# Kernel tuning notes

Measured on AMD Instinct MI355X. Metric: run time of the kernel, lower is better.

The kernel has to match this reference:

```python
import jax, jax.numpy as jnp
import numpy as np

B, S, D, H, DFF = 2, 2048, 1024, 16, 4096
DK = D // H
EPS = 1e-6
MASK_FILL = -1.0  # original code uses -1**9 == -1 (precedence bug), NOT -1e9


def layernorm(x, gamma, beta):
    # original: (x - mean) / (std + eps), std unbiased (torch default ddof=1), scalar gamma/beta
    mean = jnp.mean(x, axis=-1, keepdims=True)
    std = jnp.std(x, axis=-1, keepdims=True, ddof=1)
    return gamma * (x - mean) / (std + EPS) + beta


def setup_inputs() -> dict:
    key = jax.random.key(0)
    ks = jax.random.split(key, 12)
    sc = 0.02
    return {
        "x": jax.random.normal(ks[0], (B, S, D), jnp.float32),
        "src_mask": jnp.ones((B, 1, 1, S), jnp.int32),
        "wq": jax.random.normal(ks[1], (D, D), jnp.float32) * sc,
        "bq": jnp.zeros((D,), jnp.float32),
        "wk": jax.random.normal(ks[2], (D, D), jnp.float32) * sc,
        "bk": jnp.zeros((D,), jnp.float32),
        "wv": jax.random.normal(ks[3], (D, D), jnp.float32) * sc,
        "bv": jnp.zeros((D,), jnp.float32),
        "wo": jax.random.normal(ks[4], (D, D), jnp.float32) * sc,
        "bo": jnp.zeros((D,), jnp.float32),
        "w1": jax.random.normal(ks[5], (D, DFF), jnp.float32) * sc,
        "b1": jnp.zeros((DFF,), jnp.float32),
        "w2": jax.random.normal(ks[6], (DFF, D), jnp.float32) * sc,
        "b2": jnp.zeros((D,), jnp.float32),
        "g1": jnp.ones((), jnp.float32),
        "be1": jnp.zeros((), jnp.float32),
        "g2": jnp.ones((), jnp.float32),
        "be2": jnp.zeros((), jnp.float32),
    }


def reference(x, src_mask, wq, bq, wk, bk, wv, bv, wo, bo,
              w1, b1, w2, b2, g1, be1, g2, be2):
    # --- residual 1: pre-LN self-attention ---
    xn = layernorm(x, g1, be1)
    q = (xn @ wq + bq).reshape(B, S, H, DK).transpose(0, 2, 1, 3)  # [B,H,S,DK]
    k = (xn @ wk + bk).reshape(B, S, H, DK).transpose(0, 2, 1, 3)
    v = (xn @ wv + bv).reshape(B, S, H, DK).transpose(0, 2, 1, 3)
    scores = jnp.einsum('bhqd,bhkd->bhqk', q, k) / jnp.sqrt(jnp.float32(DK))
    scores = jnp.where(src_mask == 0, MASK_FILL, scores)
    attn = jax.nn.softmax(scores, axis=-1)
    ctx = jnp.einsum('bhqk,bhkd->bhqd', attn, v)
    ctx = ctx.transpose(0, 2, 1, 3).reshape(B, S, D)
    attn_out = ctx @ wo + bo
    x = x + attn_out  # dropout is identity in eval

    # --- residual 2: pre-LN feed-forward ---
    xn = layernorm(x, g2, be2)
    h = jax.nn.relu(xn @ w1 + b1)
    ff_out = h @ w2 + b2
    return x + ff_out
```

## Files before the change

kernel.cpp:

```cpp
#include <hip/hip_runtime.h>

typedef unsigned short u16;
typedef __bf16 bf16x8 __attribute__((ext_vector_type(8)));
typedef float f32x4 __attribute__((ext_vector_type(4)));
typedef float f32x16 __attribute__((ext_vector_type(16)));

#define AS1U(p) ((__attribute__((address_space(1))) unsigned int*)(p))
#define AS3U(p) ((__attribute__((address_space(3))) unsigned int*)(p))

__device__ __forceinline__ u16 f2bf(float f) {
  union { float f; unsigned int i; } c; c.f = f;
  return (u16)((c.i + 0x7FFFu + ((c.i >> 16) & 1u)) >> 16);
}
__device__ __forceinline__ u16 f2bf_trunc(float f) {
  union { float f; unsigned int i; } c; c.f = f;
  return (u16)(c.i >> 16);
}
__device__ __forceinline__ unsigned cvt_pk_bf16(float lo, float hi) {
  unsigned r;
  asm("v_cvt_pk_bf16_f32 %0, %1, %2" : "=v"(r) : "v"(lo), "v"(hi));
  return r;
}
__device__ __forceinline__ void plswap(unsigned& a, unsigned& b) {
  asm("v_permlane32_swap_b32 %0, %1" : "+v"(a), "+v"(b));
}

template <int OMODE>
__global__ __launch_bounds__(512, 2) void gemm8(
    const u16* __restrict__ A, long lda,
    const u16* __restrict__ B, long ldb,
    void* __restrict__ Cv, long ldc,
    int K, const float* __restrict__ bias,
    const float* __restrict__ res, long ldres, int relu) {
  __shared__ u16 As[2][256 * 64];
  __shared__ u16 Bs[2][256 * 64];
  const int t = threadIdx.x;
  const int w = t >> 6, l = t & 63;
  const int hi = l >> 5, lq = l & 31;
  const int wm = w >> 2, wn = w & 3;
  const long row0 = (long)blockIdx.x * 256;
  const long col0 = (long)blockIdx.y * 256;

  auto stageU = [&](int bb, int unit, int k0) {
    const u16* src = (unit < 2) ? B : A;
    const long ld = (unit < 2) ? ldb : lda;
    const long base0 = (unit < 2) ? col0 : row0;
    u16* dst = (unit < 2) ? &Bs[bb][0] : &As[bb][0];
    const int h = unit & 1;
#pragma unroll
    for (int i = 0; i < 2; i++) {
      int s = t + i * 512;
      int r = h * 128 + (s >> 3), c = s & 7;
      __builtin_amdgcn_global_load_lds(AS1U(src + (base0 + r) * ld + k0 + ((c ^ (r & 7)) * 8)),
                                       AS3U(dst + ((long)(r * 8 + c)) * 8), 16, 0, 0);
    }
  };

  f32x16 acc[4][2] = {};
  const int NT = K >> 6;

  stageU(0, 0, 0); stageU(0, 1, 0); stageU(0, 2, 0); stageU(0, 3, 0);
  if (NT > 1) stageU(1, 0, 64);
  asm volatile("s_waitcnt vmcnt(2)" ::: "memory");
  __builtin_amdgcn_sched_barrier(0);
  __builtin_amdgcn_s_barrier();
  __builtin_amdgcn_sched_barrier(0);

  bf16x8 bfr[2][4];
  for (int tt = 0; tt < NT; tt++) {
    const int cb = tt & 1, nb = cb ^ 1;
    const int kN = (tt + 1) << 6, kN2 = (tt + 2) << 6;
#pragma unroll
    for (int mi = 0; mi < 4; mi++) {
      bf16x8 afr[4];
      {
        const int r = wm * 128 + mi * 32 + lq;
#pragma unroll
        for (int kk = 0; kk < 4; kk++)
          afr[kk] = *(const bf16x8*)&As[cb][(r * 8 + ((kk * 2 + hi) ^ (r & 7))) * 8];
      }
      if (mi == 0) {
#pragma unroll
        for (int nj = 0; nj < 2; nj++) {
          const int r = wn * 64 + nj * 32 + lq;
#pragma unroll
          for (int kk = 0; kk < 4; kk++)
            bfr[nj][kk] = *(const bf16x8*)&Bs[cb][(r * 8 + ((kk * 2 + hi) ^ (r & 7))) * 8];
        }
      }
      if (mi == 0) { if (tt + 1 < NT) stageU(nb, 1, kN); }
      else if (mi == 1) { if (tt + 1 < NT) stageU(nb, 2, kN); }
      else if (mi == 2) { if (tt + 1 < NT) stageU(nb, 3, kN); }
      else {
        if (tt + 2 < NT) stageU(cb, 0, kN2);
        if (tt < NT - 2) asm volatile("s_waitcnt vmcnt(2)" ::: "memory");
        else             asm volatile("s_waitcnt vmcnt(0)" ::: "memory");
      }
      __builtin_amdgcn_sched_barrier(0);
      __builtin_amdgcn_s_barrier();
      __builtin_amdgcn_sched_barrier(0);
      __builtin_amdgcn_s_setprio(1);
#pragma unroll
      for (int kk = 0; kk < 4; kk++)
#pragma unroll
        for (int nj = 0; nj < 2; nj++)
          acc[mi][nj] = __builtin_amdgcn_mfma_f32_32x32x16_bf16(afr[kk], bfr[nj][kk], acc[mi][nj], 0, 0, 0);
      __builtin_amdgcn_s_setprio(0);
      __builtin_amdgcn_sched_barrier(0);
      __builtin_amdgcn_s_barrier();
      __builtin_amdgcn_sched_barrier(0);
    }
  }

#pragma unroll
  for (int nj = 0; nj < 2; nj++) {
    const long gn = col0 + wn * 64 + nj * 32 + lq;
    const float bv = bias ? bias[gn] : 0.0f;
#pragma unroll
    for (int mi = 0; mi < 4; mi++) {
#pragma unroll
      for (int g = 0; g < 16; g++) {
        const long gm = row0 + wm * 128 + mi * 32 + (g & 3) + 8 * (g >> 2) + 4 * hi;
        float v = acc[mi][nj][g] + bv;
        if (relu && v < 0.0f) v = 0.0f;
        if (res) v += res[gm * ldres + gn];
        if (OMODE == 0) ((float*)Cv)[gm * ldc + gn] = v;
        else ((u16*)Cv)[gm * ldc + gn] = f2bf(v);
      }
    }
  }
}

template <int BM, int BN, int BK, int OMODE>
__global__ __launch_bounds__(256) void gemm_bt(
    const u16* __restrict__ A, long lda,
    const u16* __restrict__ B, long ldb,
    void* __restrict__ Cv, long ldc,
    int K, float scale, const float* __restrict__ bias,
    const float* __restrict__ res, long ldres, int relu) {
  constexpr int WN = (BN == 128) ? 64 : 32;
  constexpr int MI = 4, NJ = WN / 16;
  constexpr int KK = BK / 32;
  __shared__ u16 As0[BM * BK], As1[BM * BK];
  __shared__ u16 Bs0[BN * BK], Bs1[BN * BK];
  const int t = threadIdx.x;
  const int w = t >> 6, l = t & 63;
  const int wr = w >> 1, wc = w & 1;
  const int quad = l >> 4, mlo = l & 15;
  const long row0 = (long)blockIdx.x * BM;
  const long col0 = (long)blockIdx.y * BN;

  f32x4 acc[MI][NJ] = {};

  auto stage = [&](u16 (&Ad)[BM * BK], u16 (&Bd)[BN * BK], int k0) {
    if (BK == 32) {
#pragma unroll
      for (int i = 0; i < BM / 64; i++) {
        int s = t + i * 256, r = s >> 2, c = s & 3;
        const u16* g = A + (row0 + r) * lda + k0 + c * 8;
        __builtin_amdgcn_global_load_lds(AS1U(g), AS3U(&Ad[s * 8]), 16, 0, 0);
      }
#pragma unroll
      for (int i = 0; i < BN / 64; i++) {
        int s = t + i * 256, r = s >> 2, c = s & 3;
        const u16* g = B + (col0 + r) * ldb + k0 + c * 8;
        __builtin_amdgcn_global_load_lds(AS1U(g), AS3U(&Bd[s * 8]), 16, 0, 0);
      }
    } else {
#pragma unroll
      for (int i = 0; i < BM / 32; i++) {
        int s = t + i * 256, r = s >> 3, c = s & 7;
        const u16* g = A + (row0 + r) * lda + k0 + (c ^ (r & 7)) * 8;
        __builtin_amdgcn_global_load_lds(AS1U(g), AS3U(&Ad[s * 8]), 16, 0, 0);
      }
#pragma unroll
      for (int i = 0; i < BN / 32; i++) {
        int s = t + i * 256, r = s >> 3, c = s & 7;
        const u16* g = B + (col0 + r) * ldb + k0 + (c ^ (r & 7)) * 8;
        __builtin_amdgcn_global_load_lds(AS1U(g), AS3U(&Bd[s * 8]), 16, 0, 0);
      }
    }
  };
  auto compute = [&](const u16 (&Asr)[BM * BK], const u16 (&Bsr)[BN * BK]) {
#pragma unroll
    for (int kk = 0; kk < KK; kk++) {
      bf16x8 a[MI], b[NJ];
#pragma unroll
      for (int i = 0; i < MI; i++) {
        int r = wr * 64 + i * 16 + mlo;
        a[i] = (BK == 32) ? *(const bf16x8*)&Asr[(r * 4 + quad) * 8]
                          : *(const bf16x8*)&Asr[(r * 8 + ((kk * 4 + quad) ^ (r & 7))) * 8];
      }
#pragma unroll
      for (int j = 0; j < NJ; j++) {
        int r = wc * WN + j * 16 + mlo;
        b[j] = (BK == 32) ? *(const bf16x8*)&Bsr[(r * 4 + quad) * 8]
                          : *(const bf16x8*)&Bsr[(r * 8 + ((kk * 4 + quad) ^ (r & 7))) * 8];
      }
#pragma unroll
      for (int i = 0; i < MI; i++)
#pragma unroll
        for (int j = 0; j < NJ; j++)
          acc[i][j] = __builtin_amdgcn_mfma_f32_16x16x32_bf16(a[i], b[j], acc[i][j], 0, 0, 0);
    }
  };

  stage(As0, Bs0, 0);
  for (int k0 = 0; k0 < K; k0 += 2 * BK) {
    __syncthreads();
    stage(As1, Bs1, k0 + BK);
    compute(As0, Bs0);
    __syncthreads();
    if (k0 + 2 * BK < K) stage(As0, Bs0, k0 + 2 * BK);
    compute(As1, Bs1);
  }

#pragma unroll
  for (int i = 0; i < MI; i++) {
#pragma unroll
    for (int j = 0; j < NJ; j++) {
      const long gn = col0 + wc * WN + j * 16 + mlo;
      const float bv = bias ? bias[gn] : 0.0f;
#pragma unroll
      for (int r = 0; r < 4; r++) {
        const long gm = row0 + wr * 64 + i * 16 + quad * 4 + r;
        float v = acc[i][j][r] * scale + bv;
        if (relu && v < 0.0f) v = 0.0f;
        if (res) v += res[gm * ldres + gn];
        if (OMODE == 0) ((float*)Cv)[gm * ldc + gn] = v;
        else ((u16*)Cv)[gm * ldc + gn] = f2bf(v);
      }
    }
  }
}

__global__ __launch_bounds__(256, 2) void flash_attn(
    const u16* __restrict__ QKV, const u16* __restrict__ VT,
    const int* __restrict__ mask, u16* __restrict__ ctx) {
  __shared__ u16 Ks[2][64 * 64];
  __shared__ u16 Vs[2][64 * 64];
  const int t = threadIdx.x;
  const int w = t >> 6, l = t & 63;
  const int hi = l >> 5, lq = l & 31, rx = lq & 7;
  const int z = blockIdx.z, b = z >> 4, h = z & 15;
  const long q0 = (long)blockIdx.x * 128;
  const u16* Qg = QKV + (long)b * (2048L * 3072) + h * 64;
  const u16* Kg = Qg + 1024;
  const u16* Vg = VT + (long)b * (1024L * 2048) + (long)(h * 64) * 2048;
  const int* mrow = mask + b * 2048;

#pragma unroll
  for (int i = 0; i < 2; i++) {
    int s = t + i * 256, r = s >> 3, c = s & 7;
    __builtin_amdgcn_global_load_lds(AS1U(Kg + (long)r * 3072 + (c ^ (r & 7)) * 8),
                                     AS3U(&Ks[0][s * 8]), 16, 0, 0);
    __builtin_amdgcn_global_load_lds(AS1U(Vg + (long)r * 2048 + (c ^ (r & 7)) * 8),
                                     AS3U(&Vs[0][s * 8]), 16, 0, 0);
  }

  const float CS = 0.125f * 1.44269504f;
  const float CM = -1.44269504f;

  bf16x8 aq[4];
#pragma unroll
  for (int kk = 0; kk < 4; kk++) {
    const u16* g = Qg + (q0 + w * 32 + lq) * 3072 + kk * 16 + hi * 8;
    union { uint4 u; bf16x8 v; u16 s[8]; } cc; cc.u = *(const uint4*)g;
#pragma unroll
    for (int e = 0; e < 8; e++) {
      union { unsigned u; float f; } qf; qf.u = (unsigned)cc.s[e] << 16;
      cc.s[e] = f2bf(qf.f * CS);
    }
    aq[kk] = cc.v;
  }

  unsigned am = 0;
  for (int it = 0; it < 32; ++it) {
    unsigned long long bmv = __ballot(mrow[it * 64 + l] != 0);
    am |= ((bmv == ~0ull) ? 1u : 0u) << it;
  }

  f32x16 o[2] = {}, den = {};
  union { u16 s[8]; bf16x8 v; } ones;
#pragma unroll
  for (int e = 0; e < 8; e++) ones.s[e] = 0x3F80;

  for (int it = 0; it < 32; ++it) {
    const int cur = it & 1;
    __syncthreads();
    if (it + 1 < 32) {
      const int nb = 1 - cur;
      const u16* Kg2 = Kg + (long)(it + 1) * 64 * 3072;
      const u16* Vg2 = Vg + (it + 1) * 64;
#pragma unroll
      for (int i2 = 0; i2 < 2; i2++) {
        int s = t + i2 * 256, r = s >> 3, c = s & 7;
        __builtin_amdgcn_global_load_lds(AS1U(Kg2 + (long)r * 3072 + (c ^ (r & 7)) * 8),
                                         AS3U(&Ks[nb][s * 8]), 16, 0, 0);
        __builtin_amdgcn_global_load_lds(AS1U(Vg2 + (long)r * 2048 + (c ^ (r & 7)) * 8),
                                         AS3U(&Vs[nb][s * 8]), 16, 0, 0);
      }
    }
    const bool allone = (am >> it) & 1u;
    unsigned long long bm = ~0ull;
    if (!allone) bm = __ballot(mrow[it * 64 + l] != 0);

    f32x16 sa[2];
    __builtin_amdgcn_s_setprio(1);
#pragma unroll
    for (int kt = 0; kt < 2; kt++) {
      f32x16 s0 = {};
      const int rk = kt * 32 + lq;
#pragma unroll
      for (int kk = 0; kk < 4; kk++) {
        bf16x8 ak = *(const bf16x8*)&Ks[cur][(rk * 8 + ((2 * kk + hi) ^ rx)) * 8];
        s0 = __builtin_amdgcn_mfma_f32_32x32x16_bf16(ak, aq[kk], s0, 0, 0, 0);
      }
      sa[kt] = s0;
    }
    __builtin_amdgcn_s_setprio(0);

#pragma unroll
    for (int kt = 0; kt < 2; kt++) {
      float p[16];
      if (allone) {
#pragma unroll
        for (int g = 0; g < 16; g++) p[g] = __builtin_amdgcn_exp2f(sa[kt][g]);
      } else {
#pragma unroll
        for (int g = 0; g < 16; g++) {
          const int k = kt * 32 + (g & 3) + 8 * (g >> 2) + 4 * hi;
          const float s = ((bm >> k) & 1) ? sa[kt][g] : CM;
          p[g] = __builtin_amdgcn_exp2f(s);
        }
      }
      unsigned wd[4][2];
#pragma unroll
      for (int g = 0; g < 4; g++) {
        wd[g][0] = cvt_pk_bf16(p[4 * g + 0], p[4 * g + 1]);
        wd[g][1] = cvt_pk_bf16(p[4 * g + 2], p[4 * g + 3]);
      }
#pragma unroll
      for (int c = 0; c < 2; c++) {
        plswap(wd[2 * c][0], wd[2 * c + 1][0]);
        plswap(wd[2 * c][1], wd[2 * c + 1][1]);
        union { unsigned u[4]; bf16x8 v; } pa;
        pa.u[0] = wd[2 * c][0];
        pa.u[1] = wd[2 * c][1];
        pa.u[2] = wd[2 * c + 1][0];
        pa.u[3] = wd[2 * c + 1][1];
        const int cg = kt * 2 + c;
        __builtin_amdgcn_s_setprio(1);
#pragma unroll
        for (int dt = 0; dt < 2; dt++) {
          const int rv = dt * 32 + lq;
          bf16x8 bv = *(const bf16x8*)&Vs[cur][(rv * 8 + ((2 * cg + hi) ^ rx)) * 8];
          o[dt] = __builtin_amdgcn_mfma_f32_32x32x16_bf16(pa.v, bv, o[dt], 0, 0, 0);
        }
        den = __builtin_amdgcn_mfma_f32_32x32x16_bf16(pa.v, ones.v, den, 0, 0, 0);
        __builtin_amdgcn_s_setprio(0);
      }
    }
  }

  u16* cb = ctx + (long)b * (2048L * 1024) + (q0 + w * 32) * 1024 + h * 64;
#pragma unroll
  for (int g = 0; g < 16; g++) {
    const int row = (g & 3) + 8 * (g >> 2) + 4 * hi;
    const float inv = 1.0f / den[g];
    cb[(long)row * 1024 + lq] = f2bf(o[0][g] * inv);
    cb[(long)row * 1024 + 32 + lq] = f2bf(o[1][g] * inv);
  }
}

__device__ __forceinline__ void ln_row(const float* __restrict__ x, u16* __restrict__ y,
                                       const float* __restrict__ g, const float* __restrict__ b,
                                       long row, float* ss, float* s2) {
  const float* xr = x + row * 1024;
  float v[4];
  float s = 0.f, sq = 0.f;
#pragma unroll
  for (int i = 0; i < 4; i++) {
    float f = xr[threadIdx.x + i * 256];
    v[i] = f; s += f; sq += f * f;
  }
#pragma unroll
  for (int o = 32; o > 0; o >>= 1) { s += __shfl_xor(s, o, 64); sq += __shfl_xor(sq, o, 64); }
  const int w = threadIdx.x >> 6;
  if ((threadIdx.x & 63) == 0) { ss[w] = s; s2[w] = sq; }
  __syncthreads();
  s = ss[0] + ss[1] + ss[2] + ss[3];
  sq = s2[0] + s2[1] + s2[2] + s2[3];
  const float mean = s * (1.0f / 1024.0f);
  float var = (sq - s * mean) * (1.0f / 1023.0f);
  var = fmaxf(var, 0.0f);
  const float sc = g[0] / (sqrtf(var) + 1e-6f);
  const float be = b[0];
#pragma unroll
  for (int i = 0; i < 4; i++)
    y[row * 1024 + threadIdx.x + i * 256] = f2bf((v[i] - mean) * sc + be);
}

__global__ __launch_bounds__(256) void ln_kernel(const float* __restrict__ x, u16* __restrict__ y,
                                                 const float* __restrict__ g, const float* __restrict__ b) {
  __shared__ float ss[4], s2[4];
  ln_row(x, y, g, b, blockIdx.x, ss, s2);
}

__global__ __launch_bounds__(256) void prep_kernel(
    const float* __restrict__ x, const float* __restrict__ g1, const float* __restrict__ be1,
    const float* __restrict__ wq, const float* __restrict__ wk, const float* __restrict__ wv,
    const float* __restrict__ wo, const float* __restrict__ w1, const float* __restrict__ w2,
    const float* __restrict__ bq, const float* __restrict__ bk, const float* __restrict__ bv,
    u16* __restrict__ xnH, u16* __restrict__ WqkvT, u16* __restrict__ woT,
    u16* __restrict__ w1T, u16* __restrict__ w2T, float* __restrict__ biasQKV) {
  __shared__ float tile[32][33];
  __shared__ float ss[4], s2[4];
  const int bid = blockIdx.x;
  if (bid >= 12300) {
    ln_row(x, xnH, g1, be1, bid - 12300, ss, s2);
    return;
  }
  if (bid >= 12288) {
    const int i = (bid - 12288) * 256 + threadIdx.x;
    if (i < 3072) biasQKV[i] = (i < 1024) ? bq[i] : ((i < 2048) ? bk[i - 1024] : bv[i - 2048]);
    return;
  }
  const float* in; u16* out; long ldin, ldo; int ti, tiles_x;
  if (bid < 1024)      { in = wq; out = WqkvT;                     ldin = 1024; ldo = 1024; ti = bid;        tiles_x = 32; }
  else if (bid < 2048) { in = wk; out = WqkvT + (size_t)1024*1024; ldin = 1024; ldo = 1024; ti = bid - 1024; tiles_x = 32; }
  else if (bid < 3072) { in = wv; out = WqkvT + (size_t)2048*1024; ldin = 1024; ldo = 1024; ti = bid - 2048; tiles_x = 32; }
  else if (bid < 4096) { in = wo; out = woT;                       ldin = 1024; ldo = 1024; ti = bid - 3072; tiles_x = 32; }
  else if (bid < 8192) { in = w1; out = w1T;                       ldin = 4096; ldo = 1024; ti = bid - 4096; tiles_x = 128; }
  else                 { in = w2; out = w2T;                       ldin = 1024; ldo = 4096; ti = bid - 8192; tiles_x = 32; }
  const int bx = (ti % tiles_x) * 32, by = (ti / tiles_x) * 32;
  const int tx = threadIdx.x & 31, ty = threadIdx.x >> 5;
#pragma unroll
  for (int i = 0; i < 32; i += 8) tile[ty + i][tx] = in[(long)(by + ty + i) * ldin + bx + tx];
  __syncthreads();
#pragma unroll
  for (int i = 0; i < 32; i += 8)
    out[(long)(bx + ty + i) * ldo + by + tx] = f2bf(tile[tx][ty + i]);
}

__global__ __launch_bounds__(256) void ttrans1(const u16* __restrict__ in, long ldin, long siz,
                                               u16* __restrict__ out, long ldo, long soz) {
  __shared__ u16 tile[32][33];
  const long zi = (long)blockIdx.z * siz, zo = (long)blockIdx.z * soz;
  const int bx = blockIdx.x * 32, by = blockIdx.y * 32;
  const int tx = threadIdx.x & 31, ty = threadIdx.x >> 5;
#pragma unroll
  for (int i = 0; i < 32; i += 8)
    tile[ty + i][tx] = in[zi + (long)(by + ty + i) * ldin + bx + tx];
  __syncthreads();
#pragma unroll
  for (int i = 0; i < 32; i += 8)
    out[zo + (long)(bx + ty + i) * ldo + by + tx] = tile[tx][ty + i];
}

extern "C" void kernel_launch(void* const* d_in, const int* in_sizes, int n_in,
                              void* d_out, int out_size, void* d_ws, size_t ws_size,
                              hipStream_t stream) {
  const float* x   = (const float*)d_in[0];
  const int*   msk = (const int*)d_in[1];
  const float* wq  = (const float*)d_in[2];
  const float* bq  = (const float*)d_in[3];
  const float* wk  = (const float*)d_in[4];
  const float* bk  = (const float*)d_in[5];
  const float* wv  = (const float*)d_in[6];
  const float* bv  = (const float*)d_in[7];
  const float* wo  = (const float*)d_in[8];
  const float* bo  = (const float*)d_in[9];
  const float* w1  = (const float*)d_in[10];
  const float* b1  = (const float*)d_in[11];
  const float* w2  = (const float*)d_in[12];
  const float* b2  = (const float*)d_in[13];
  const float* g1  = (const float*)d_in[14];
  const float* be1 = (const float*)d_in[15];
  const float* g2  = (const float*)d_in[16];
  const float* be2 = (const float*)d_in[17];
  float* out = (float*)d_out;

  char* basep = (char*)d_ws;
  size_t off = 0;
  auto au = [&](size_t nelem) -> u16* {
    u16* r = (u16*)(basep + off);
    off += ((nelem * 2) + 255) & ~(size_t)255;
    return r;
  };
  auto afp = [&](size_t nelem) -> float* {
    float* r = (float*)(basep + off);
    off += ((nelem * 4) + 255) & ~(size_t)255;
    return r;
  };

  u16* xnH  = au((size_t)4096 * 1024);
  u16* QKV  = au((size_t)4096 * 3072);
  u16* VTH  = au((size_t)2 * 1024 * 2048);
  u16* ctxH = au((size_t)4096 * 1024);
  float* x1 = afp((size_t)4096 * 1024);
  u16* hb   = au((size_t)4096 * 4096);
  u16* WqkvT = au((size_t)3072 * 1024);
  u16* woT  = au((size_t)1024 * 1024);
  u16* w1T  = au((size_t)4096 * 1024);
  u16* w2T  = au((size_t)1024 * 4096);
  float* biasQKV = afp(3072);

  const dim3 blk(256);
  const dim3 blk5(512);

  prep_kernel<<<16396, blk, 0, stream>>>(x, g1, be1, wq, wk, wv, wo, w1, w2,
                                         bq, bk, bv, xnH, WqkvT, woT, w1T, w2T, biasQKV);

  gemm8<2><<<dim3(16, 12), blk5, 0, stream>>>(
      xnH, 1024, WqkvT, 1024, QKV, 3072, 1024,
      biasQKV, (const float*)0, 0, 0);

  ttrans1<<<dim3(32, 64, 2), blk, 0, stream>>>(
      QKV + 2048, 3072, (long)2048 * 3072, VTH, 2048, (long)1024 * 2048);

  flash_attn<<<dim3(16, 1, 32), blk, 0, stream>>>(QKV, VTH, msk, ctxH);

  gemm_bt<128, 64, 64, 0><<<dim3(32, 16), blk, 0, stream>>>(
      ctxH, 1024, woT, 1024, x1, 1024, 1024, 1.0f, bo, x, 1024, 0);

  ln_kernel<<<4096, blk, 0, stream>>>(x1, xnH, g2, be2);

  gemm8<2><<<dim3(16, 16), blk5, 0, stream>>>(
      xnH, 1024, w1T, 1024, hb, 4096, 1024,
      b1, (const float*)0, 0, 1);

  gemm_bt<128, 64, 64, 0><<<dim3(32, 16), blk, 0, stream>>>(
      hb, 4096, w2T, 4096, out, 1024, 4096, 1.0f, b2, x1, 1024, 0);
}
```

Measured before the change: 343.1 us.

## Replace N=1024 GEMMs with 256x128 32x32-MFMA kernel and split-K FFN2

Replaces the generic gemm_bt kernel with a 512-thread, 256x128-tile kernel built on 32x32x16 MFMA, with staggered A/B staging, barriers and setprio, used for the output projection and the second FFN GEMM. The FFN2 GEMM becomes split-K by two, writing fp32 partials into the now-unused QKV buffer, and a new elementwise kernel sums the partials with bias and residual. The aim is higher MFMA throughput and enough blocks (256) to fill the CUs for the small-N GEMMs. The cost is an extra partials round trip through memory and an extra launch.

```diff
diff --git a/kernel.cpp b/kernel.cpp
--- a/kernel.cpp
+++ b/kernel.cpp
@@ -11,10 +11,6 @@
 __device__ __forceinline__ u16 f2bf(float f) {
   union { float f; unsigned int i; } c; c.f = f;
   return (u16)((c.i + 0x7FFFu + ((c.i >> 16) & 1u)) >> 16);
-}
-__device__ __forceinline__ u16 f2bf_trunc(float f) {
-  union { float f; unsigned int i; } c; c.f = f;
-  return (u16)(c.i >> 16);
 }
 __device__ __forceinline__ unsigned cvt_pk_bf16(float lo, float hi) {
   unsigned r;
@@ -131,107 +127,144 @@
   }
 }
 
-template <int BM, int BN, int BK, int OMODE>
-__global__ __launch_bounds__(256) void gemm_bt(
+template <int OMODE>
+__global__ __launch_bounds__(512) void gemm8n(
     const u16* __restrict__ A, long lda,
     const u16* __restrict__ B, long ldb,
-    void* __restrict__ Cv, long ldc,
-    int K, float scale, const float* __restrict__ bias,
+    void* __restrict__ Cv, long ldc, long M,
+    int K, const float* __restrict__ bias,
     const float* __restrict__ res, long ldres, int relu) {
-  constexpr int WN = (BN == 128) ? 64 : 32;
-  constexpr int MI = 4, NJ = WN / 16;
-  constexpr int KK = BK / 32;
-  __shared__ u16 As0[BM * BK], As1[BM * BK];
-  __shared__ u16 Bs0[BN * BK], Bs1[BN * BK];
+  __shared__ u16 As[2][256 * 64];
+  __shared__ u16 Bs[2][128 * 64];
   const int t = threadIdx.x;
   const int w = t >> 6, l = t & 63;
-  const int wr = w >> 1, wc = w & 1;
-  const int quad = l >> 4, mlo = l & 15;
-  const long row0 = (long)blockIdx.x * BM;
-  const long col0 = (long)blockIdx.y * BN;
-
-  f32x4 acc[MI][NJ] = {};
-
-  auto stage = [&](u16 (&Ad)[BM * BK], u16 (&Bd)[BN * BK], int k0) {
-    if (BK == 32) {
-#pragma unroll
-      for (int i = 0; i < BM / 64; i++) {
-        int s = t + i * 256, r = s >> 2, c = s & 3;
-        const u16* g = A + (row0 + r) * lda + k0 + c * 8;
-        __builtin_amdgcn_global_load_lds(AS1U(g), AS3U(&Ad[s * 8]), 16, 0, 0);
-      }
-#pragma unroll
-      for (int i = 0; i < BN / 64; i++) {
-        int s = t + i * 256, r = s >> 2, c = s & 3;
-        const u16* g = B + (col0 + r) * ldb + k0 + c * 8;
-        __builtin_amdgcn_global_load_lds(AS1U(g), AS3U(&Bd[s * 8]), 16, 0, 0);
-      }
+  const int hi = l >> 5, lq = l & 31;
+  const int wm = w >> 1, wn = w & 1;
+  const long col0 = (long)blockIdx.x * 128;
+  const long row0 = (long)blockIdx.y * 256;
+  const int koff = blockIdx.z * K;
+
+  auto stageA = [&](int bb, int k0) {
+#pragma unroll
+    for (int i = 0; i < 4; i++) {
+      int s = t + i * 512, r = s >> 3, c = s & 7;
+      __builtin_amdgcn_global_load_lds(AS1U(A + (row0 + r) * lda + k0 + ((c ^ (r & 7)) * 8)),
+                                       AS3U(&As[bb][0] + ((long)(r * 8 + c)) * 8), 16, 0, 0);
+    }
+  };
+  auto stageB = [&](int bb, int k0) {
+#pragma unroll
+    for (int i = 0; i < 2; i++) {
+      int s = t + i * 512, r = s >> 3, c = s & 7;
+      __builtin_amdgcn_global_load_lds(AS1U(B + (col0 + r) * ldb + k0 + ((c ^ (r & 7)) * 8)),
+                                       AS3U(&Bs[bb][0] + ((long)(r * 8 + c)) * 8), 16, 0, 0);
+    }
+  };
+
+  f32x16 acc[2][2] = {};
+  const int NT = K >> 6;
+
+  stageA(0, koff); stageB(0, koff);
+  stageB(1, koff + 64);
+  asm volatile("s_waitcnt vmcnt(2)" ::: "memory");
+  __builtin_amdgcn_sched_barrier(0);
+  __builtin_amdgcn_s_barrier();
+  __builtin_amdgcn_sched_barrier(0);
+
+  bf16x8 bfr[2][4];
+  for (int tt = 0; tt < NT; tt++) {
+    const int cb = tt & 1, nb = cb ^ 1;
+    bf16x8 a0[4];
+    {
+      const int r = wm * 64 + lq;
+#pragma unroll
+      for (int kk = 0; kk < 4; kk++)
+        a0[kk] = *(const bf16x8*)&As[cb][(r * 8 + ((kk * 2 + hi) ^ (r & 7))) * 8];
+    }
+#pragma unroll
+    for (int nj = 0; nj < 2; nj++) {
+      const int r = wn * 64 + nj * 32 + lq;
+#pragma unroll
+      for (int kk = 0; kk < 4; kk++)
+        bfr[nj][kk] = *(const bf16x8*)&Bs[cb][(r * 8 + ((kk * 2 + hi) ^ (r & 7))) * 8];
+    }
+    if (tt + 1 < NT) stageA(nb, koff + ((tt + 1) << 6));
+    __builtin_amdgcn_sched_barrier(0);
+    __builtin_amdgcn_s_barrier();
+    __builtin_amdgcn_sched_barrier(0);
+    __builtin_amdgcn_s_setprio(1);
+#pragma unroll
+    for (int kk = 0; kk < 4; kk++)
+#pragma unroll
+      for (int nj = 0; nj < 2; nj++)
+        acc[0][nj] = __builtin_amdgcn_mfma_f32_32x32x16_bf16(a0[kk], bfr[nj][kk], acc[0][nj], 0, 0, 0);
+    __builtin_amdgcn_s_setprio(0);
+    __builtin_amdgcn_sched_barrier(0);
+    __builtin_amdgcn_s_barrier();
+    __builtin_amdgcn_sched_barrier(0);
+    bf16x8 a1[4];
+    {
+      const int r = wm * 64 + 32 + lq;
+#pragma unroll
+      for (int kk = 0; kk < 4; kk++)
+        a1[kk] = *(const bf16x8*)&As[cb][(r * 8 + ((kk * 2 + hi) ^ (r & 7))) * 8];
+    }
+    if (tt + 2 < NT) {
+      stageB(cb, koff + ((tt + 2) << 6));
+      asm volatile("s_waitcnt vmcnt(2)" ::: "memory");
     } else {
-#pragma unroll
-      for (int i = 0; i < BM / 32; i++) {
-        int s = t + i * 256, r = s >> 3, c = s & 7;
-        const u16* g = A + (row0 + r) * lda + k0 + (c ^ (r & 7)) * 8;
-        __builtin_amdgcn_global_load_lds(AS1U(g), AS3U(&Ad[s * 8]), 16, 0, 0);
-      }
-#pragma unroll
-      for (int i = 0; i < BN / 32; i++) {
-        int s = t + i * 256, r = s >> 3, c = s & 7;
-        const u16* g = B + (col0 + r) * ldb + k0 + (c ^ (r & 7)) * 8;
-        __builtin_amdgcn_global_load_lds(AS1U(g), AS3U(&Bd[s * 8]), 16, 0, 0);
-      }
-    }
-  };
-  auto compute = [&](const u16 (&Asr)[BM * BK], const u16 (&Bsr)[BN * BK]) {
-#pragma unroll
-    for (int kk = 0; kk < KK; kk++) {
-      bf16x8 a[MI], b[NJ];
-#pragma unroll
-      for (int i = 0; i < MI; i++) {
-        int r = wr * 64 + i * 16 + mlo;
-        a[i] = (BK == 32) ? *(const bf16x8*)&Asr[(r * 4 + quad) * 8]
-                          : *(const bf16x8*)&Asr[(r * 8 + ((kk * 4 + quad) ^ (r & 7))) * 8];
-      }
-#pragma unroll
-      for (int j = 0; j < NJ; j++) {
-        int r = wc * WN + j * 16 + mlo;
-        b[j] = (BK == 32) ? *(const bf16x8*)&Bsr[(r * 4 + quad) * 8]
-                          : *(const bf16x8*)&Bsr[(r * 8 + ((kk * 4 + quad) ^ (r & 7))) * 8];
-      }
-#pragma unroll
-      for (int i = 0; i < MI; i++)
-#pragma unroll
-        for (int j = 0; j < NJ; j++)
-          acc[i][j] = __builtin_amdgcn_mfma_f32_16x16x32_bf16(a[i], b[j], acc[i][j], 0, 0, 0);
-    }
-  };
-
-  stage(As0, Bs0, 0);
-  for (int k0 = 0; k0 < K; k0 += 2 * BK) {
-    __syncthreads();
-    stage(As1, Bs1, k0 + BK);
-    compute(As0, Bs0);
-    __syncthreads();
-    if (k0 + 2 * BK < K) stage(As0, Bs0, k0 + 2 * BK);
-    compute(As1, Bs1);
-  }
-
-#pragma unroll
-  for (int i = 0; i < MI; i++) {
-#pragma unroll
-    for (int j = 0; j < NJ; j++) {
-      const long gn = col0 + wc * WN + j * 16 + mlo;
-      const float bv = bias ? bias[gn] : 0.0f;
-#pragma unroll
-      for (int r = 0; r < 4; r++) {
-        const long gm = row0 + wr * 64 + i * 16 + quad * 4 + r;
-        float v = acc[i][j][r] * scale + bv;
+      asm volatile("s_waitcnt vmcnt(0)" ::: "memory");
+    }
+    __builtin_amdgcn_sched_barrier(0);
+    __builtin_amdgcn_s_barrier();
+    __builtin_amdgcn_sched_barrier(0);
+    __builtin_amdgcn_s_setprio(1);
+#pragma unroll
+    for (int kk = 0; kk < 4; kk++)
+#pragma unroll
+      for (int nj = 0; nj < 2; nj++)
+        acc[1][nj] = __builtin_amdgcn_mfma_f32_32x32x16_bf16(a1[kk], bfr[nj][kk], acc[1][nj], 0, 0, 0);
+    __builtin_amdgcn_s_setprio(0);
+    __builtin_amdgcn_sched_barrier(0);
+    __builtin_amdgcn_s_barrier();
+    __builtin_amdgcn_sched_barrier(0);
+  }
+
+  float* Cz = (float*)Cv + (long)blockIdx.z * M * ldc;
+#pragma unroll
+  for (int nj = 0; nj < 2; nj++) {
+    const long gn = col0 + wn * 64 + nj * 32 + lq;
+    const float bv = bias ? bias[gn] : 0.0f;
+#pragma unroll
+    for (int mi = 0; mi < 2; mi++) {
+#pragma unroll
+      for (int g = 0; g < 16; g++) {
+        const long gm = row0 + wm * 64 + mi * 32 + (g & 3) + 8 * (g >> 2) + 4 * hi;
+        float v = acc[mi][nj][g] + bv;
         if (relu && v < 0.0f) v = 0.0f;
         if (res) v += res[gm * ldres + gn];
-        if (OMODE == 0) ((float*)Cv)[gm * ldc + gn] = v;
+        if (OMODE == 0) Cz[gm * ldc + gn] = v;
         else ((u16*)Cv)[gm * ldc + gn] = f2bf(v);
       }
     }
   }
+}
+
+__global__ __launch_bounds__(256) void ffn2_fin(
+    const float* __restrict__ p, const float* __restrict__ x1,
+    const float* __restrict__ b2, float* __restrict__ out) {
+  const long idx = (long)blockIdx.x * 256 + threadIdx.x;
+  const float4 a = ((const float4*)x1)[idx];
+  const float4 b = ((const float4*)b2)[threadIdx.x & 255 ? (idx & 255) : (idx & 255)];
+  const float4 q0 = ((const float4*)p)[idx];
+  const float4 q1 = ((const float4*)p)[idx + (long)4096 * 256];
+  float4 r;
+  const float4 bb = ((const float4*)b2)[idx & 255];
+  r.x = a.x + bb.x + q0.x + q1.x;
+  r.y = a.y + bb.y + q0.y + q1.y;
+  r.z = a.z + bb.z + q0.z + q1.z;
+  r.w = a.w + bb.w + q0.w + q1.w;
+  ((float4*)out)[idx] = r;
 }
 
 __global__ __launch_bounds__(256, 2) void flash_attn(
@@ -505,6 +538,7 @@
   u16* w1T  = au((size_t)4096 * 1024);
   u16* w2T  = au((size_t)1024 * 4096);
   float* biasQKV = afp(3072);
+  float* Pp = (float*)QKV;
 
   const dim3 blk(256);
   const dim3 blk5(512);
@@ -521,8 +555,8 @@
 
   flash_attn<<<dim3(16, 1, 32), blk, 0, stream>>>(QKV, VTH, msk, ctxH);
 
-  gemm_bt<128, 64, 64, 0><<<dim3(32, 16), blk, 0, stream>>>(
-      ctxH, 1024, woT, 1024, x1, 1024, 1024, 1.0f, bo, x, 1024, 0);
+  gemm8n<0><<<dim3(8, 16, 1), blk5, 0, stream>>>(
+      ctxH, 1024, woT, 1024, x1, 1024, 4096, 1024, bo, x, 1024, 0);
 
   ln_kernel<<<4096, blk, 0, stream>>>(x1, xnH, g2, be2);
 
@@ -530,6 +564,9 @@
       xnH, 1024, w1T, 1024, hb, 4096, 1024,
       b1, (const float*)0, 0, 1);
 
-  gemm_bt<128, 64, 64, 0><<<dim3(32, 16), blk, 0, stream>>>(
-      hb, 4096, w2T, 4096, out, 1024, 4096, 1.0f, b2, x1, 1024, 0);
-}
+  gemm8n<0><<<dim3(8, 16, 2), blk5, 0, stream>>>(
+      hb, 4096, w2T, 4096, Pp, 1024, 4096, 2048,
+      (const float*)0, (const float*)0, 0, 0);
+
+  ffn2_fin<<<4096, blk, 0, stream>>>(Pp, x1, b2, out);
+}
```

Result: slower. 371.7 us (+8.3%).

## Split-K FFN2 GEMM with large-tile kernel and separate reduction epilogue

Applied to the files above, without the earlier changes.

Replaces the FFN down-projection (K=4096) gemm_bt launch with the 256x256-tile gemm8 kernel using a 4-way split-K over blockIdx.z. Each split writes fp32 partials into a buffer that reuses the QKV workspace region. A new elementwise kernel then sums the four partials and adds bias and residual. The aim is to use the faster large-tile MFMA kernel while keeping enough blocks (256) in flight. The cost is an extra 64MB of fp32 partial writes and reads plus one more launch.

```diff
diff --git a/kernel.cpp b/kernel.cpp
--- a/kernel.cpp
+++ b/kernel.cpp
@@ -12,10 +12,6 @@
   union { float f; unsigned int i; } c; c.f = f;
   return (u16)((c.i + 0x7FFFu + ((c.i >> 16) & 1u)) >> 16);
 }
-__device__ __forceinline__ u16 f2bf_trunc(float f) {
-  union { float f; unsigned int i; } c; c.f = f;
-  return (u16)(c.i >> 16);
-}
 __device__ __forceinline__ unsigned cvt_pk_bf16(float lo, float hi) {
   unsigned r;
   asm("v_cvt_pk_bf16_f32 %0, %1, %2" : "=v"(r) : "v"(lo), "v"(hi));
@@ -29,7 +25,7 @@
 __global__ __launch_bounds__(512, 2) void gemm8(
     const u16* __restrict__ A, long lda,
     const u16* __restrict__ B, long ldb,
-    void* __restrict__ Cv, long ldc,
+    void* __restrict__ Cv, long ldc, long zstride,
     int K, const float* __restrict__ bias,
     const float* __restrict__ res, long ldres, int relu) {
   __shared__ u16 As[2][256 * 64];
@@ -40,6 +36,7 @@
   const int wm = w >> 2, wn = w & 3;
   const long row0 = (long)blockIdx.x * 256;
   const long col0 = (long)blockIdx.y * 256;
+  const int koff = blockIdx.z * K;
 
   auto stageU = [&](int bb, int unit, int k0) {
     const u16* src = (unit < 2) ? B : A;
@@ -51,7 +48,7 @@
     for (int i = 0; i < 2; i++) {
       int s = t + i * 512;
       int r = h * 128 + (s >> 3), c = s & 7;
-      __builtin_amdgcn_global_load_lds(AS1U(src + (base0 + r) * ld + k0 + ((c ^ (r & 7)) * 8)),
+      __builtin_amdgcn_global_load_lds(AS1U(src + (base0 + r) * ld + koff + k0 + ((c ^ (r & 7)) * 8)),
                                        AS3U(dst + ((long)(r * 8 + c)) * 8), 16, 0, 0);
     }
   };
@@ -112,6 +109,7 @@
     }
   }
 
+  float* Cf = (float*)Cv + (long)blockIdx.z * zstride;
 #pragma unroll
   for (int nj = 0; nj < 2; nj++) {
     const long gn = col0 + wn * 64 + nj * 32 + lq;
@@ -124,7 +122,7 @@
         float v = acc[mi][nj][g] + bv;
         if (relu && v < 0.0f) v = 0.0f;
         if (res) v += res[gm * ldres + gn];
-        if (OMODE == 0) ((float*)Cv)[gm * ldc + gn] = v;
+        if (OMODE == 0) Cf[gm * ldc + gn] = v;
         else ((u16*)Cv)[gm * ldc + gn] = f2bf(v);
       }
     }
@@ -153,32 +151,17 @@
   f32x4 acc[MI][NJ] = {};
 
   auto stage = [&](u16 (&Ad)[BM * BK], u16 (&Bd)[BN * BK], int k0) {
-    if (BK == 32) {
-#pragma unroll
-      for (int i = 0; i < BM / 64; i++) {
-        int s = t + i * 256, r = s >> 2, c = s & 3;
-        const u16* g = A + (row0 + r) * lda + k0 + c * 8;
-        __builtin_amdgcn_global_load_lds(AS1U(g), AS3U(&Ad[s * 8]), 16, 0, 0);
-      }
-#pragma unroll
-      for (int i = 0; i < BN / 64; i++) {
-        int s = t + i * 256, r = s >> 2, c = s & 3;
-        const u16* g = B + (col0 + r) * ldb + k0 + c * 8;
-        __builtin_amdgcn_global_load_lds(AS1U(g), AS3U(&Bd[s * 8]), 16, 0, 0);
-      }
-    } else {
-#pragma unroll
-      for (int i = 0; i < BM / 32; i++) {
-        int s = t + i * 256, r = s >> 3, c = s & 7;
-        const u16* g = A + (row0 + r) * lda + k0 + (c ^ (r & 7)) * 8;
-        __builtin_amdgcn_global_load_lds(AS1U(g), AS3U(&Ad[s * 8]), 16, 0, 0);
-      }
-#pragma unroll
-      for (int i = 0; i < BN / 32; i++) {
-        int s = t + i * 256, r = s >> 3, c = s & 7;
-        const u16* g = B + (col0 + r) * ldb + k0 + (c ^ (r & 7)) * 8;
-        __builtin_amdgcn_global_load_lds(AS1U(g), AS3U(&Bd[s * 8]), 16, 0, 0);
-      }
+#pragma unroll
+    for (int i = 0; i < BM / 32; i++) {
+      int s = t + i * 256, r = s >> 3, c = s & 7;
+      const u16* g = A + (row0 + r) * lda + k0 + (c ^ (r & 7)) * 8;
+      __builtin_amdgcn_global_load_lds(AS1U(g), AS3U(&Ad[s * 8]), 16, 0, 0);
+    }
+#pragma unroll
+    for (int i = 0; i < BN / 32; i++) {
+      int s = t + i * 256, r = s >> 3, c = s & 7;
+      const u16* g = B + (col0 + r) * ldb + k0 + (c ^ (r & 7)) * 8;
+      __builtin_amdgcn_global_load_lds(AS1U(g), AS3U(&Bd[s * 8]), 16, 0, 0);
     }
   };
   auto compute = [&](const u16 (&Asr)[BM * BK], const u16 (&Bsr)[BN * BK]) {
@@ -188,14 +171,12 @@
 #pragma unroll
       for (int i = 0; i < MI; i++) {
         int r = wr * 64 + i * 16 + mlo;
-        a[i] = (BK == 32) ? *(const bf16x8*)&Asr[(r * 4 + quad) * 8]
-                          : *(const bf16x8*)&Asr[(r * 8 + ((kk * 4 + quad) ^ (r & 7))) * 8];
+        a[i] = *(const bf16x8*)&Asr[(r * 8 + ((kk * 4 + quad) ^ (r & 7))) * 8];
       }
 #pragma unroll
       for (int j = 0; j < NJ; j++) {
         int r = wc * WN + j * 16 + mlo;
-        b[j] = (BK == 32) ? *(const bf16x8*)&Bsr[(r * 4 + quad) * 8]
-                          : *(const bf16x8*)&Bsr[(r * 8 + ((kk * 4 + quad) ^ (r & 7))) * 8];
+        b[j] = *(const bf16x8*)&Bsr[(r * 8 + ((kk * 4 + quad) ^ (r & 7))) * 8];
       }
 #pragma unroll
       for (int i = 0; i < MI; i++)
@@ -232,6 +213,24 @@
       }
     }
   }
+}
+
+__global__ __launch_bounds__(256) void ffn2_fin(
+    const float* __restrict__ p, const float* __restrict__ x1,
+    const float* __restrict__ b2, float* __restrict__ out) {
+  const long idx = (long)blockIdx.x * 256 + threadIdx.x;
+  const float4 a = ((const float4*)x1)[idx];
+  const float4 bb = ((const float4*)b2)[idx & 255];
+  const float4 q0 = ((const float4*)p)[idx];
+  const float4 q1 = ((const float4*)p)[idx + 1048576];
+  const float4 q2 = ((const float4*)p)[idx + 2097152];
+  const float4 q3 = ((const float4*)p)[idx + 3145728];
+  float4 r;
+  r.x = a.x + bb.x + ((q0.x + q1.x) + (q2.x + q3.x));
+  r.y = a.y + bb.y + ((q0.y + q1.y) + (q2.y + q3.y));
+  r.z = a.z + bb.z + ((q0.z + q1.z) + (q2.z + q3.z));
+  r.w = a.w + bb.w + ((q0.w + q1.w) + (q2.w + q3.w));
+  ((float4*)out)[idx] = r;
 }
 
 __global__ __launch_bounds__(256, 2) void flash_attn(
@@ -494,17 +493,18 @@
     return r;
   };
 
-  u16* xnH  = au((size_t)4096 * 1024);
   u16* QKV  = au((size_t)4096 * 3072);
   u16* VTH  = au((size_t)2 * 1024 * 2048);
+  u16* xnH  = au((size_t)4096 * 1024);
   u16* ctxH = au((size_t)4096 * 1024);
-  float* x1 = afp((size_t)4096 * 1024);
-  u16* hb   = au((size_t)4096 * 4096);
   u16* WqkvT = au((size_t)3072 * 1024);
   u16* woT  = au((size_t)1024 * 1024);
   u16* w1T  = au((size_t)4096 * 1024);
+  float* x1 = afp((size_t)4096 * 1024);
+  u16* hb   = au((size_t)4096 * 4096);
   u16* w2T  = au((size_t)1024 * 4096);
   float* biasQKV = afp(3072);
+  float* Pp = (float*)QKV;
 
   const dim3 blk(256);
   const dim3 blk5(512);
@@ -512,8 +512,8 @@
   prep_kernel<<<16396, blk, 0, stream>>>(x, g1, be1, wq, wk, wv, wo, w1, w2,
                                          bq, bk, bv, xnH, WqkvT, woT, w1T, w2T, biasQKV);
 
-  gemm8<2><<<dim3(16, 12), blk5, 0, stream>>>(
-      xnH, 1024, WqkvT, 1024, QKV, 3072, 1024,
+  gemm8<2><<<dim3(16, 12, 1), blk5, 0, stream>>>(
+      xnH, 1024, WqkvT, 1024, QKV, 3072, 0, 1024,
       biasQKV, (const float*)0, 0, 0);
 
   ttrans1<<<dim3(32, 64, 2), blk, 0, stream>>>(
@@ -526,10 +526,13 @@
 
   ln_kernel<<<4096, blk, 0, stream>>>(x1, xnH, g2, be2);
 
-  gemm8<2><<<dim3(16, 16), blk5, 0, stream>>>(
-      xnH, 1024, w1T, 1024, hb, 4096, 1024,
+  gemm8<2><<<dim3(16, 16, 1), blk5, 0, stream>>>(
+      xnH, 1024, w1T, 1024, hb, 4096, 0, 1024,
       b1, (const float*)0, 0, 1);
 
-  gemm_bt<128, 64, 64, 0><<<dim3(32, 16), blk, 0, stream>>>(
-      hb, 4096, w2T, 4096, out, 1024, 4096, 1.0f, b2, x1, 1024, 0);
-}
+  gemm8<0><<<dim3(16, 4, 4), blk5, 0, stream>>>(
+      hb, 4096, w2T, 4096, Pp, 1024, (long)4096 * 1024, 1024,
+      (const float*)0, (const float*)0, 0, 0);
+
+  ffn2_fin<<<4096, blk, 0, stream>>>(Pp, x1, b2, out);
+}
```

Result: slower. 352.4 us (+2.7%).

## Split attention over two key halves and combine partials in a finalize kernel

Applied to the files above, without the earlier changes.

The flash attention kernel now splits the key/value sequence into two halves along a new grid dimension. This doubles the block count, and the occupancy hint is raised to 4 blocks per CU. Each split writes unnormalized fp32 output and denominator partials into reused workspace buffers. A new ctx_fin kernel sums the two halves, normalizes, and writes the bf16 context. This works only because the kernel uses no running max, and it adds extra global traffic plus a kernel launch. The unused BK==32 path in the tiled GEMM is also removed.

```diff
diff --git a/kernel.cpp b/kernel.cpp
--- a/kernel.cpp
+++ b/kernel.cpp
@@ -11,10 +11,6 @@
 __device__ __forceinline__ u16 f2bf(float f) {
   union { float f; unsigned int i; } c; c.f = f;
   return (u16)((c.i + 0x7FFFu + ((c.i >> 16) & 1u)) >> 16);
-}
-__device__ __forceinline__ u16 f2bf_trunc(float f) {
-  union { float f; unsigned int i; } c; c.f = f;
-  return (u16)(c.i >> 16);
 }
 __device__ __forceinline__ unsigned cvt_pk_bf16(float lo, float hi) {
   unsigned r;
@@ -153,32 +149,17 @@
   f32x4 acc[MI][NJ] = {};
 
   auto stage = [&](u16 (&Ad)[BM * BK], u16 (&Bd)[BN * BK], int k0) {
-    if (BK == 32) {
-#pragma unroll
-      for (int i = 0; i < BM / 64; i++) {
-        int s = t + i * 256, r = s >> 2, c = s & 3;
-        const u16* g = A + (row0 + r) * lda + k0 + c * 8;
-        __builtin_amdgcn_global_load_lds(AS1U(g), AS3U(&Ad[s * 8]), 16, 0, 0);
-      }
-#pragma unroll
-      for (int i = 0; i < BN / 64; i++) {
-        int s = t + i * 256, r = s >> 2, c = s & 3;
-        const u16* g = B + (col0 + r) * ldb + k0 + c * 8;
-        __builtin_amdgcn_global_load_lds(AS1U(g), AS3U(&Bd[s * 8]), 16, 0, 0);
-      }
-    } else {
-#pragma unroll
-      for (int i = 0; i < BM / 32; i++) {
-        int s = t + i * 256, r = s >> 3, c = s & 7;
-        const u16* g = A + (row0 + r) * lda + k0 + (c ^ (r & 7)) * 8;
-        __builtin_amdgcn_global_load_lds(AS1U(g), AS3U(&Ad[s * 8]), 16, 0, 0);
-      }
-#pragma unroll
-      for (int i = 0; i < BN / 32; i++) {
-        int s = t + i * 256, r = s >> 3, c = s & 7;
-        const u16* g = B + (col0 + r) * ldb + k0 + (c ^ (r & 7)) * 8;
-        __builtin_amdgcn_global_load_lds(AS1U(g), AS3U(&Bd[s * 8]), 16, 0, 0);
-      }
+#pragma unroll
+    for (int i = 0; i < BM / 32; i++) {
+      int s = t + i * 256, r = s >> 3, c = s & 7;
+      const u16* g = A + (row0 + r) * lda + k0 + (c ^ (r & 7)) * 8;
+      __builtin_amdgcn_global_load_lds(AS1U(g), AS3U(&Ad[s * 8]), 16, 0, 0);
+    }
+#pragma unroll
+    for (int i = 0; i < BN / 32; i++) {
+      int s = t + i * 256, r = s >> 3, c = s & 7;
+      const u16* g = B + (col0 + r) * ldb + k0 + (c ^ (r & 7)) * 8;
+      __builtin_amdgcn_global_load_lds(AS1U(g), AS3U(&Bd[s * 8]), 16, 0, 0);
     }
   };
   auto compute = [&](const u16 (&Asr)[BM * BK], const u16 (&Bsr)[BN * BK]) {
@@ -188,14 +169,12 @@
 #pragma unroll
       for (int i = 0; i < MI; i++) {
         int r = wr * 64 + i * 16 + mlo;
-        a[i] = (BK == 32) ? *(const bf16x8*)&Asr[(r * 4 + quad) * 8]
-                          : *(const bf16x8*)&Asr[(r * 8 + ((kk * 4 + quad) ^ (r & 7))) * 8];
+        a[i] = *(const bf16x8*)&Asr[(r * 8 + ((kk * 4 + quad) ^ (r & 7))) * 8];
       }
 #pragma unroll
       for (int j = 0; j < NJ; j++) {
         int r = wc * WN + j * 16 + mlo;
-        b[j] = (BK == 32) ? *(const bf16x8*)&Bsr[(r * 4 + quad) * 8]
-                          : *(const bf16x8*)&Bsr[(r * 8 + ((kk * 4 + quad) ^ (r & 7))) * 8];
+        b[j] = *(const bf16x8*)&Bsr[(r * 8 + ((kk * 4 + quad) ^ (r & 7))) * 8];
       }
 #pragma unroll
       for (int i = 0; i < MI; i++)
@@ -234,20 +213,22 @@
   }
 }
 
-__global__ __launch_bounds__(256, 2) void flash_attn(
+__global__ __launch_bounds__(256, 4) void flash_attn(
     const u16* __restrict__ QKV, const u16* __restrict__ VT,
-    const int* __restrict__ mask, u16* __restrict__ ctx) {
+    const int* __restrict__ mask, float* __restrict__ oP,
+    float* __restrict__ denP) {
   __shared__ u16 Ks[2][64 * 64];
   __shared__ u16 Vs[2][64 * 64];
   const int t = threadIdx.x;
   const int w = t >> 6, l = t & 63;
   const int hi = l >> 5, lq = l & 31, rx = lq & 7;
+  const int y = blockIdx.y;
   const int z = blockIdx.z, b = z >> 4, h = z & 15;
   const long q0 = (long)blockIdx.x * 128;
   const u16* Qg = QKV + (long)b * (2048L * 3072) + h * 64;
-  const u16* Kg = Qg + 1024;
-  const u16* Vg = VT + (long)b * (1024L * 2048) + (long)(h * 64) * 2048;
-  const int* mrow = mask + b * 2048;
+  const u16* Kg = Qg + 1024 + (long)(y * 1024) * 3072;
+  const u16* Vg = VT + (long)b * (1024L * 2048) + (long)(h * 64) * 2048 + y * 1024;
+  const int* mrow = mask + b * 2048 + y * 1024;
 
 #pragma unroll
   for (int i = 0; i < 2; i++) {
@@ -275,7 +256,7 @@
   }
 
   unsigned am = 0;
-  for (int it = 0; it < 32; ++it) {
+  for (int it = 0; it < 16; ++it) {
     unsigned long long bmv = __ballot(mrow[it * 64 + l] != 0);
     am |= ((bmv == ~0ull) ? 1u : 0u) << it;
   }
@@ -285,10 +266,10 @@
 #pragma unroll
   for (int e = 0; e < 8; e++) ones.s[e] = 0x3F80;
 
-  for (int it = 0; it < 32; ++it) {
+  for (int it = 0; it < 16; ++it) {
     const int cur = it & 1;
     __syncthreads();
-    if (it + 1 < 32) {
+    if (it + 1 < 16) {
       const int nb = 1 - cur;
       const u16* Kg2 = Kg + (long)(it + 1) * 64 * 3072;
       const u16* Vg2 = Vg + (it + 1) * 64;
@@ -363,14 +344,37 @@
     }
   }
 
-  u16* cb = ctx + (long)b * (2048L * 1024) + (q0 + w * 32) * 1024 + h * 64;
+  float* ob = oP + (((long)(y * 2 + b) * 16 + h) * 2048 + q0 + w * 32) * 64;
 #pragma unroll
   for (int g = 0; g < 16; g++) {
     const int row = (g & 3) + 8 * (g >> 2) + 4 * hi;
-    const float inv = 1.0f / den[g];
-    cb[(long)row * 1024 + lq] = f2bf(o[0][g] * inv);
-    cb[(long)row * 1024 + 32 + lq] = f2bf(o[1][g] * inv);
-  }
+    ob[(long)row * 64 + lq] = o[0][g];
+    ob[(long)row * 64 + 32 + lq] = o[1][g];
+  }
+  if (lq == 0) {
+    float* db = denP + ((long)(y * 2 + b) * 16 + h) * 2048 + q0 + w * 32;
+#pragma unroll
+    for (int g = 0; g < 16; g++)
+      db[(g & 3) + 8 * (g >> 2) + 4 * hi] = den[g];
+  }
+}
+
+__global__ __launch_bounds__(256) void ctx_fin(
+    const float* __restrict__ oP, const float* __restrict__ denP,
+    u16* __restrict__ ctx) {
+  const int r = blockIdx.x;
+  const int b = r >> 11, q = r & 2047;
+  const int c = threadIdx.x * 4;
+  const int h = c >> 6, d = c & 63;
+  const long base = (((long)b * 16 + h) * 2048 + q) * 64 + d;
+  const long half = (long)2 * 16 * 2048 * 64;
+  const float4 a0 = *(const float4*)(oP + base);
+  const float4 a1 = *(const float4*)(oP + base + half);
+  const long dbase = ((long)b * 16 + h) * 2048 + q;
+  const float inv = 1.0f / (denP[dbase] + denP[dbase + (long)2 * 16 * 2048]);
+  u16 ov[4] = { f2bf((a0.x + a1.x) * inv), f2bf((a0.y + a1.y) * inv),
+                f2bf((a0.z + a1.z) * inv), f2bf((a0.w + a1.w) * inv) };
+  *(uint2*)(ctx + (long)r * 1024 + c) = *(uint2*)ov;
 }
 
 __device__ __forceinline__ void ln_row(const float* __restrict__ x, u16* __restrict__ y,
@@ -494,17 +498,20 @@
     return r;
   };
 
-  u16* xnH  = au((size_t)4096 * 1024);
   u16* QKV  = au((size_t)4096 * 3072);
   u16* VTH  = au((size_t)2 * 1024 * 2048);
+  u16* xnH  = au((size_t)4096 * 1024);
   u16* ctxH = au((size_t)4096 * 1024);
-  float* x1 = afp((size_t)4096 * 1024);
-  u16* hb   = au((size_t)4096 * 4096);
   u16* WqkvT = au((size_t)3072 * 1024);
   u16* woT  = au((size_t)1024 * 1024);
   u16* w1T  = au((size_t)4096 * 1024);
+  float* x1 = afp((size_t)4096 * 1024);
+  u16* hb   = au((size_t)4096 * 4096);
   u16* w2T  = au((size_t)1024 * 4096);
   float* biasQKV = afp(3072);
+
+  float* oP   = x1;
+  float* denP = (float*)WqkvT;
 
   const dim3 blk(256);
   const dim3 blk5(512);
@@ -519,7 +526,9 @@
   ttrans1<<<dim3(32, 64, 2), blk, 0, stream>>>(
       QKV + 2048, 3072, (long)2048 * 3072, VTH, 2048, (long)1024 * 2048);
 
-  flash_attn<<<dim3(16, 1, 32), blk, 0, stream>>>(QKV, VTH, msk, ctxH);
+  flash_attn<<<dim3(16, 2, 32), blk, 0, stream>>>(QKV, VTH, msk, oP, denP);
+
+  ctx_fin<<<4096, blk, 0, stream>>>(oP, denP, ctxH);
 
   gemm_bt<128, 64, 64, 0><<<dim3(32, 16), blk, 0, stream>>>(
       ctxH, 1024, woT, 1024, x1, 1024, 1024, 1.0f, bo, x, 1024, 0);
```

Measured after the change: 404.1 us. 17.8% more time.
